# Kernel optimization log

Measured on AMD Instinct MI355X. Metric: run time of the kernel, lower is better.

Reference implementation:

```python
import jax, jax.numpy as jnp
import numpy as np

D_MODEL = 1024
N_HEADS = 16
D_HEAD = D_MODEL // N_HEADS
D_FF = 4096
EPS = 1e-5
NEG = -1e10


def setup_inputs() -> dict:
    key = jax.random.key(0)
    ks = jax.random.split(key, 16)
    s = 0.02
    x = jax.random.normal(ks[0], (4, 1024, D_MODEL), dtype=jnp.float32)
    mask = jnp.ones((4, 1, 1, 1024), dtype=jnp.int32)
    return {
        "x": x,
        "mask": mask,
        "Wq": jax.random.normal(ks[1], (D_MODEL, D_MODEL), jnp.float32) * s,
        "Wk": jax.random.normal(ks[2], (D_MODEL, D_MODEL), jnp.float32) * s,
        "Wv": jax.random.normal(ks[3], (D_MODEL, D_MODEL), jnp.float32) * s,
        "Wp": jax.random.normal(ks[4], (D_MODEL, D_MODEL), jnp.float32) * s,
        "bp": jnp.zeros((D_MODEL,), jnp.float32),
        "W1": jax.random.normal(ks[5], (D_MODEL, D_FF), jnp.float32) * s,
        "b1": jnp.zeros((D_FF,), jnp.float32),
        "W2": jax.random.normal(ks[6], (D_FF, D_MODEL), jnp.float32) * s,
        "b2": jnp.zeros((D_MODEL,), jnp.float32),
        "g1": jnp.ones((D_MODEL,), jnp.float32),
        "be1": jnp.zeros((D_MODEL,), jnp.float32),
        "g2": jnp.ones((D_MODEL,), jnp.float32),
        "be2": jnp.zeros((D_MODEL,), jnp.float32),
    }


def _layer_norm(x, g, b):
    mu = jnp.mean(x, axis=-1, keepdims=True)
    var = jnp.mean(jnp.square(x - mu), axis=-1, keepdims=True)
    return (x - mu) * jax.lax.rsqrt(var + EPS) * g + b


def _mha(x, mask, Wq, Wk, Wv, Wp, bp):
    B, L, _ = x.shape
    q = (x @ Wq).reshape(B, L, N_HEADS, D_HEAD).transpose(0, 2, 1, 3)  # (B,H,L,dh)
    k = (x @ Wk).reshape(B, L, N_HEADS, D_HEAD).transpose(0, 2, 1, 3)
    v = (x @ Wv).reshape(B, L, N_HEADS, D_HEAD).transpose(0, 2, 1, 3)
    scores = jnp.einsum('bhqd,bhkd->bhqk', q, k) / jnp.sqrt(jnp.float32(D_HEAD))
    scores = jnp.where(mask == 0, NEG, scores)
    attn = jax.nn.softmax(scores, axis=-1)
    heads = jnp.einsum('bhqk,bhkd->bhqd', attn, v)  # (B,H,L,dh)
    heads = heads.transpose(0, 2, 1, 3).reshape(B, L, D_MODEL)
    return heads @ Wp + bp


def reference(x, mask, Wq, Wk, Wv, Wp, bp, W1, b1, W2, b2, g1, be1, g2, be2):
    # Post-norm residual sublayers (dropout inactive at inference)
    attn_out = _mha(x, mask, Wq, Wk, Wv, Wp, bp)
    h = _layer_norm(x + attn_out, g1, be1)
    ff = jax.nn.relu(h @ W1 + b1) @ W2 + b2
    out = _layer_norm(h + ff, g2, be2)
    return out
```

## Files before the change

### kernel.cpp

```cpp
#include <hip/hip_runtime.h>
#include <hip/hip_bf16.h>

typedef __attribute__((ext_vector_type(8))) short short8;
typedef __attribute__((ext_vector_type(4))) short short4v;
typedef __attribute__((ext_vector_type(4))) float float4v;

static __device__ __forceinline__ float b2f(short s) {
    return __builtin_bit_cast(float, ((unsigned)(unsigned short)s) << 16);
}
static __device__ __forceinline__ short f2b(float f) {
    unsigned x = __builtin_bit_cast(unsigned, f);
    unsigned r = (x + 0x7fffu + ((x >> 16) & 1u)) >> 16;
    return (short)r;
}
static __device__ __forceinline__ void gload_lds16(const short* g, short* l) {
    __builtin_amdgcn_global_load_lds(
        (const __attribute__((address_space(1))) void*)g,
        (__attribute__((address_space(3))) void*)l, 16, 0, 0);
}

static __device__ __forceinline__ void tile_transpose(const float* __restrict__ in,
                                                      short* __restrict__ out,
                                                      int R, int C, int bx, int by,
                                                      float tile[64][65])
{
    const int tx = threadIdx.x;
    const int r0 = by * 64, c0 = bx * 64;
    const int lr = tx >> 4, lc = (tx & 15) * 4;
#pragma unroll
    for (int p = 0; p < 4; p++) {
        const float4v v = *(const float4v*)&in[(size_t)(r0 + lr + p * 16) * C + c0 + lc];
#pragma unroll
        for (int j = 0; j < 4; j++) tile[lr + p * 16][lc + j] = v[j];
    }
    __syncthreads();
    const int oc = tx >> 3, orr = (tx & 7) * 8;
#pragma unroll
    for (int p = 0; p < 2; p++) {
        const int c = oc + p * 32;
        short8 pk;
#pragma unroll
        for (int j = 0; j < 8; j++) pk[j] = f2b(tile[orr + j][c]);
        *(short8*)&out[(size_t)(c0 + c) * R + r0 + orr] = pk;
    }
}

__global__ __launch_bounds__(256) void prep_k(const float* __restrict__ x,
                                              const float* __restrict__ Wq,
                                              const float* __restrict__ Wk,
                                              const float* __restrict__ Wv,
                                              const float* __restrict__ Wp,
                                              const float* __restrict__ W1,
                                              const float* __restrict__ W2,
                                              short* __restrict__ xb,
                                              short* __restrict__ WqkvT,
                                              short* __restrict__ WpT,
                                              short* __restrict__ W1T,
                                              short* __restrict__ W2T)
{
    __shared__ float tile[64][65];
    const int b = blockIdx.x;
    if (b < 4096) {
        const size_t i = ((size_t)b * 256 + threadIdx.x) * 4;
        const float4v v = *(const float4v*)&x[i];
        short4v s;
#pragma unroll
        for (int j = 0; j < 4; j++) s[j] = f2b(v[j]);
        *(short4v*)&xb[i] = s;
    } else if (b < 5120) {
        const int lb = b - 4096;
        const int wsel = lb >> 8, t = lb & 255;
        const float* in = (wsel == 0) ? Wq : (wsel == 1) ? Wk : (wsel == 2) ? Wv : Wp;
        short* out = (wsel < 3) ? (WqkvT + ((size_t)wsel << 20)) : WpT;
        tile_transpose(in, out, 1024, 1024, t & 15, t >> 4, tile);
    } else if (b < 6144) {
        const int lb = b - 5120;
        tile_transpose(W1, W1T, 1024, 4096, lb & 63, lb >> 6, tile);
    } else {
        const int lb = b - 6144;
        tile_transpose(W2, W2T, 4096, 1024, lb & 15, lb >> 4, tile);
    }
}

template<int MODE, int BM, int BN, int KH>
__global__ __launch_bounds__(256) void gemm_bt(const short* __restrict__ X,
                                               const short* __restrict__ Wt,
                                               short* __restrict__ out,
                                               const float* __restrict__ bias,
                                               const short* __restrict__ alt,
                                               int M, int N, int K)
{
    constexpr int MI = BM / 32, NI = BN / 32;
    __shared__ short As[KH][BM * 32];
    __shared__ short Bs[KH][BN * 32];
    const int tid = threadIdx.x;
    const int wave = tid >> 6, lane = tid & 63;
    const int quad = lane >> 4, l16 = lane & 15;

    int bx = blockIdx.x, by = blockIdx.y;
    {
        const int nbx = gridDim.x, nby = gridDim.y;
        if ((nby & 7) == 0) {
            const int g = by * nbx + bx;
            const int xcd = g & 7, local = g >> 3, Y = nby >> 3;
            by = xcd * Y + (local % Y);
            bx = local / Y;
        }
    }
    const int m0 = by * BM, n0 = bx * BN;
    const int wm = (wave >> 1) * (BM / 2), wn = (wave & 1) * (BN / 2);

    int kb = 0, ke = K;
    short* op = out;
    if (MODE == 5) {
        const int ks = K / (int)gridDim.z;
        kb = blockIdx.z * ks;
        ke = kb + ks;
        op = (blockIdx.z == 3 && alt) ? const_cast<short*>(alt)
                                      : out + (size_t)blockIdx.z * M * N;
    }

    const int srow = tid >> 2;
    const int scs = (((tid & 3) ^ (srow & 3)) * 8);
    const int rg = ((l16 & 3)) * 8;

    float4v acc[MI][NI] = {};

    for (int k0 = kb; k0 < ke; k0 += KH * 32) {
#pragma unroll
        for (int c = 0; c < BM / 64; c++)
#pragma unroll
            for (int h = 0; h < KH; h++)
                gload_lds16(X + (size_t)(m0 + c * 64 + srow) * K + k0 + h * 32 + scs,
                            &As[h][(c * 256 + tid) * 8]);
#pragma unroll
        for (int c = 0; c < BN / 64; c++)
#pragma unroll
            for (int h = 0; h < KH; h++)
                gload_lds16(Wt + (size_t)(n0 + c * 64 + srow) * K + k0 + h * 32 + scs,
                            &Bs[h][(c * 256 + tid) * 8]);
        __syncthreads();
#pragma unroll
        for (int h = 0; h < KH; h++) {
            short8 af[MI], bf[NI];
#pragma unroll
            for (int i = 0; i < MI; i++)
                af[i] = *(const short8*)&As[h][(wm + i * 16 + l16) * 32 + ((quad * 8) ^ rg)];
#pragma unroll
            for (int i = 0; i < NI; i++)
                bf[i] = *(const short8*)&Bs[h][(wn + i * 16 + l16) * 32 + ((quad * 8) ^ rg)];
#pragma unroll
            for (int mi = 0; mi < MI; mi++)
#pragma unroll
                for (int ni = 0; ni < NI; ni++)
                    acc[mi][ni] = __builtin_amdgcn_mfma_f32_16x16x32_bf16(af[mi], bf[ni], acc[mi][ni], 0, 0, 0);
        }
        __syncthreads();
    }

#pragma unroll
    for (int mi = 0; mi < MI; mi++) {
#pragma unroll
        for (int ni = 0; ni < NI; ni++) {
            const int gn = n0 + wn + ni * 16 + l16;
            const float bv = (MODE == 2) ? bias[gn] : 0.0f;
#pragma unroll
            for (int r = 0; r < 4; r++) {
                const int gm = m0 + wm + mi * 16 + quad * 4 + r;
                float v = acc[mi][ni][r];
                if (MODE == 4) {
                    const int s = gn >> 10;
                    const int n = gn & 1023;
                    const int hh = n >> 6, d = n & 63;
                    const size_t bh16 = (size_t)((gm >> 10) * 16 + hh) << 16;
                    const size_t base = (size_t)s << 22;
                    if (s == 0)      out[base + bh16 + ((size_t)(gm & 1023) << 6) + d] = f2b(v * 0.125f);
                    else if (s == 1) out[base + bh16 + ((size_t)(gm & 1023) << 6) + d] = f2b(v);
                    else             out[base + bh16 + ((size_t)d << 10) + (gm & 1023)] = f2b(v);
                } else if (MODE == 2) {
                    v += bv;
                    v = fmaxf(v, 0.0f);
                    out[(size_t)gm * N + gn] = f2b(v);
                } else {
                    op[(size_t)gm * N + gn] = f2b(v);
                }
            }
        }
    }
}

__global__ __launch_bounds__(256) void attn_k(const short* __restrict__ Qb,
                                              const short* __restrict__ Kb,
                                              const short* __restrict__ Vt,
                                              const int* __restrict__ mask,
                                              short* __restrict__ heads)
{
    __shared__ short Kl[2][64 * 32];
    __shared__ short Vl[2][64 * 32];
    __shared__ short P[4][16 * 72];
    const int bh = blockIdx.x, qb = blockIdx.y;
    const int b = bh >> 4, h = bh & 15;
    const int tid = threadIdx.x, wave = tid >> 6, lane = tid & 63;
    const int quad = lane >> 4, l16 = lane & 15;
    const int qbase = qb * 64 + wave * 16;
    const short* Qp = Qb + ((size_t)bh << 16) + (size_t)qbase * 64;
    const short* Kp = Kb + ((size_t)bh << 16);
    const short* Vp = Vt + ((size_t)bh << 16);
    const int* mp = mask + (b << 10);

    const short8 bq0 = *(const short8*)&Qp[l16 * 64 + quad * 8];
    const short8 bq1 = *(const short8*)&Qp[l16 * 64 + 32 + quad * 8];

    float rs = 0.0f;
    float4v o[4] = {};
    short* myP = &P[wave][0];

    const int srow = tid >> 2, sc8 = (tid & 3) * 8;

    for (int kc = 0; kc < 1024; kc += 64) {
        gload_lds16(Kp + (size_t)(kc + srow) * 64 + sc8,      &Kl[0][tid * 8]);
        gload_lds16(Kp + (size_t)(kc + srow) * 64 + 32 + sc8, &Kl[1][tid * 8]);
        gload_lds16(Vp + (size_t)srow * 1024 + kc + sc8,      &Vl[0][tid * 8]);
        gload_lds16(Vp + (size_t)srow * 1024 + kc + 32 + sc8, &Vl[1][tid * 8]);
        __syncthreads();

        float4v s[4];
#pragma unroll
        for (int kt = 0; kt < 4; kt++) {
            s[kt] = (float4v){};
            const short8 ka = *(const short8*)&Kl[0][(kt * 16 + l16) * 32 + quad * 8];
            s[kt] = __builtin_amdgcn_mfma_f32_16x16x32_bf16(ka, bq0, s[kt], 0, 0, 0);
            const short8 kb = *(const short8*)&Kl[1][(kt * 16 + l16) * 32 + quad * 8];
            s[kt] = __builtin_amdgcn_mfma_f32_16x16x32_bf16(kb, bq1, s[kt], 0, 0, 0);
        }
#pragma unroll
        for (int kt = 0; kt < 4; kt++) {
            const int4 mv = *(const int4*)&mp[kc + kt * 16 + quad * 4];
            float p0 = mv.x ? __expf(fminf(s[kt][0], 30.f)) : 0.f;
            float p1 = mv.y ? __expf(fminf(s[kt][1], 30.f)) : 0.f;
            float p2 = mv.z ? __expf(fminf(s[kt][2], 30.f)) : 0.f;
            float p3 = mv.w ? __expf(fminf(s[kt][3], 30.f)) : 0.f;
            rs += (p0 + p1) + (p2 + p3);
            short4v w;
            w[0] = f2b(p0); w[1] = f2b(p1); w[2] = f2b(p2); w[3] = f2b(p3);
            *(short4v*)&myP[l16 * 72 + kt * 16 + quad * 4] = w;
        }
        const short8 bp0 = *(const short8*)&myP[l16 * 72 + quad * 8];
        const short8 bp1 = *(const short8*)&myP[l16 * 72 + 32 + quad * 8];
#pragma unroll
        for (int dt = 0; dt < 4; dt++) {
            const short8 va = *(const short8*)&Vl[0][(dt * 16 + l16) * 32 + quad * 8];
            o[dt] = __builtin_amdgcn_mfma_f32_16x16x32_bf16(va, bp0, o[dt], 0, 0, 0);
            const short8 vb = *(const short8*)&Vl[1][(dt * 16 + l16) * 32 + quad * 8];
            o[dt] = __builtin_amdgcn_mfma_f32_16x16x32_bf16(vb, bp1, o[dt], 0, 0, 0);
        }
        __syncthreads();
    }

    rs += __shfl_xor(rs, 16);
    rs += __shfl_xor(rs, 32);
    const float inv = 1.0f / fmaxf(rs, 1e-20f);
    const int gq = qbase + l16;
#pragma unroll
    for (int dt = 0; dt < 4; dt++) {
        short4v w;
#pragma unroll
        for (int r = 0; r < 4; r++) w[r] = f2b(o[dt][r] * inv);
        *(short4v*)&heads[((size_t)(b * 1024 + gq) << 10) + h * 64 + dt * 16 + quad * 4] = w;
    }
}

template<bool F32OUT>
__global__ __launch_bounds__(256) void red_ln_k(const short* __restrict__ p0,
                                                const short* __restrict__ p1,
                                                const short* __restrict__ p2,
                                                const short* __restrict__ p3,
                                                const float* __restrict__ bias,
                                                const short* __restrict__ res,
                                                const float* __restrict__ g,
                                                const float* __restrict__ be,
                                                short* __restrict__ outb,
                                                float* __restrict__ outf)
{
    __shared__ float red[8];
    const int row = blockIdx.x, tid = threadIdx.x;
    const size_t base = ((size_t)row << 10) + tid * 4;
    const short4v a = *(const short4v*)&p0[base];
    const short4v b = *(const short4v*)&p1[base];
    const short4v c = *(const short4v*)&p2[base];
    const short4v d = *(const short4v*)&p3[base];
    const short4v e = *(const short4v*)&res[base];
    const float4v bv = *(const float4v*)&bias[tid * 4];
    float v[4];
#pragma unroll
    for (int i = 0; i < 4; i++)
        v[i] = (b2f(a[i]) + b2f(b[i])) + (b2f(c[i]) + b2f(d[i])) + bv[i] + b2f(e[i]);
    float s = v[0] + v[1] + v[2] + v[3];
#pragma unroll
    for (int off = 32; off; off >>= 1) s += __shfl_xor(s, off);
    if ((tid & 63) == 0) red[tid >> 6] = s;
    __syncthreads();
    const float mu = (red[0] + red[1] + red[2] + red[3]) * (1.0f / 1024.0f);
    float vs = 0.f;
#pragma unroll
    for (int i = 0; i < 4; i++) { const float dd = v[i] - mu; vs += dd * dd; }
#pragma unroll
    for (int off = 32; off; off >>= 1) vs += __shfl_xor(vs, off);
    if ((tid & 63) == 0) red[4 + (tid >> 6)] = vs;
    __syncthreads();
    const float rstd = rsqrtf((red[4] + red[5] + red[6] + red[7]) * (1.0f / 1024.0f) + 1e-5f);
    const float4v gv = *(const float4v*)&g[tid * 4];
    const float4v bev = *(const float4v*)&be[tid * 4];
    if (F32OUT) {
        float4v w;
#pragma unroll
        for (int i = 0; i < 4; i++) w[i] = (v[i] - mu) * rstd * gv[i] + bev[i];
        *(float4v*)&outf[base] = w;
    } else {
        short4v w;
#pragma unroll
        for (int i = 0; i < 4; i++) w[i] = f2b((v[i] - mu) * rstd * gv[i] + bev[i]);
        *(short4v*)&outb[base] = w;
    }
}

extern "C" void kernel_launch(void* const* d_in, const int* in_sizes, int n_in,
                              void* d_out, int out_size, void* d_ws, size_t ws_size,
                              hipStream_t stream)
{
    const float* x   = (const float*)d_in[0];
    const int*   mk  = (const int*)d_in[1];
    const float* Wq  = (const float*)d_in[2];
    const float* Wk  = (const float*)d_in[3];
    const float* Wv  = (const float*)d_in[4];
    const float* Wp  = (const float*)d_in[5];
    const float* bp  = (const float*)d_in[6];
    const float* W1  = (const float*)d_in[7];
    const float* b1  = (const float*)d_in[8];
    const float* W2  = (const float*)d_in[9];
    const float* b2  = (const float*)d_in[10];
    const float* g1  = (const float*)d_in[11];
    const float* be1 = (const float*)d_in[12];
    const float* g2  = (const float*)d_in[13];
    const float* be2 = (const float*)d_in[14];
    float* out = (float*)d_out;

    char* ws = (char*)d_ws;
    const size_t MB = (size_t)1 << 20;
    short* xb     = (short*)(ws + 0 * MB);
    short* WqkvT  = (short*)(ws + 8 * MB);
    short* WpT    = (short*)(ws + 14 * MB);
    short* W1T    = (short*)(ws + 16 * MB);
    short* W2T    = (short*)(ws + 24 * MB);
    short* Qb     = (short*)(ws + 32 * MB);
    short* Kb     = (short*)(ws + 40 * MB);
    short* Vt     = (short*)(ws + 48 * MB);
    short* hd     = (short*)(ws + 56 * MB);
    short* partP  = (short*)(ws + 32 * MB);
    short* partP3 = (short*)(ws + 64 * MB);
    short* u      = (short*)(ws + 32 * MB);
    short* partF  = (short*)(ws + 0 * MB);
    short* partF3 = (short*)(ws + 64 * MB);
    short* hbuf   = (short*)(ws + 72 * MB);

    const dim3 blk(256);

    prep_k<<<dim3(7168), blk, 0, stream>>>(x, Wq, Wk, Wv, Wp, W1, W2,
                                           xb, WqkvT, WpT, W1T, W2T);

    gemm_bt<4, 128, 128, 2><<<dim3(24, 32), blk, 0, stream>>>(xb, WqkvT, Qb, nullptr, nullptr, 4096, 3072, 1024);

    attn_k<<<dim3(64, 16), blk, 0, stream>>>(Qb, Kb, Vt, mk, hd);

    gemm_bt<5, 128, 128, 2><<<dim3(8, 32, 4), blk, 0, stream>>>(hd, WpT, partP, nullptr, partP3, 4096, 1024, 1024);

    red_ln_k<false><<<dim3(4096), blk, 0, stream>>>(partP, partP + (4u << 20), partP + (8u << 20), partP3,
                                                    bp, xb, g1, be1, hbuf, nullptr);

    gemm_bt<2, 128, 128, 2><<<dim3(32, 32), blk, 0, stream>>>(hbuf, W1T, u, b1, nullptr, 4096, 4096, 1024);

    gemm_bt<5, 128, 128, 2><<<dim3(8, 32, 4), blk, 0, stream>>>(u, W2T, partF, nullptr, partF3, 4096, 1024, 4096);

    red_ln_k<true><<<dim3(4096), blk, 0, stream>>>(partF, partF + (4u << 20), partF + (8u << 20), partF3,
                                                   b2, hbuf, g2, be2, nullptr, out);
}
```

Measured before the change: 347.6 us.

## Prefetch next K/V tile into registers in attention; halve Wp split-K

The attention loop now issues global loads for the next K/V chunk into registers before computing on the current LDS tile, then writes them to LDS after the trailing barrier. This replaces direct global-to-LDS loads and is meant to overlap memory latency with the MFMA work. Separately, the output-projection GEMM uses a split-K of 2 instead of 4, and the reduce+layernorm kernel is templated on the number of partials so it reads only two partial buffers. The prefetch adds register pressure, and the smaller split reduces grid parallelism for that GEMM.

```diff
diff --git a/kernel.cpp b/kernel.cpp
--- a/kernel.cpp
+++ b/kernel.cpp
@@ -217,12 +217,23 @@
 
     const int srow = tid >> 2, sc8 = (tid & 3) * 8;
 
+    gload_lds16(Kp + (size_t)srow * 64 + sc8,        &Kl[0][tid * 8]);
+    gload_lds16(Kp + (size_t)srow * 64 + 32 + sc8,   &Kl[1][tid * 8]);
+    gload_lds16(Vp + (size_t)srow * 1024 + sc8,      &Vl[0][tid * 8]);
+    gload_lds16(Vp + (size_t)srow * 1024 + 32 + sc8, &Vl[1][tid * 8]);
+
     for (int kc = 0; kc < 1024; kc += 64) {
-        gload_lds16(Kp + (size_t)(kc + srow) * 64 + sc8,      &Kl[0][tid * 8]);
-        gload_lds16(Kp + (size_t)(kc + srow) * 64 + 32 + sc8, &Kl[1][tid * 8]);
-        gload_lds16(Vp + (size_t)srow * 1024 + kc + sc8,      &Vl[0][tid * 8]);
-        gload_lds16(Vp + (size_t)srow * 1024 + kc + 32 + sc8, &Vl[1][tid * 8]);
         __syncthreads();
+
+        short8 nk0, nk1, nv0, nv1;
+        const bool pf = (kc + 64) < 1024;
+        if (pf) {
+            const int kn = kc + 64;
+            nk0 = *(const short8*)&Kp[(size_t)(kn + srow) * 64 + sc8];
+            nk1 = *(const short8*)&Kp[(size_t)(kn + srow) * 64 + 32 + sc8];
+            nv0 = *(const short8*)&Vp[(size_t)srow * 1024 + kn + sc8];
+            nv1 = *(const short8*)&Vp[(size_t)srow * 1024 + kn + 32 + sc8];
+        }
 
         float4v s[4];
 #pragma unroll
@@ -254,7 +265,14 @@
             const short8 vb = *(const short8*)&Vl[1][(dt * 16 + l16) * 32 + quad * 8];
             o[dt] = __builtin_amdgcn_mfma_f32_16x16x32_bf16(vb, bp1, o[dt], 0, 0, 0);
         }
+
         __syncthreads();
+        if (pf) {
+            *(short8*)&Kl[0][tid * 8] = nk0;
+            *(short8*)&Kl[1][tid * 8] = nk1;
+            *(short8*)&Vl[0][tid * 8] = nv0;
+            *(short8*)&Vl[1][tid * 8] = nv1;
+        }
     }
 
     rs += __shfl_xor(rs, 16);
@@ -270,7 +288,7 @@
     }
 }
 
-template<bool F32OUT>
+template<int NP, bool F32OUT>
 __global__ __launch_bounds__(256) void red_ln_k(const short* __restrict__ p0,
                                                 const short* __restrict__ p1,
                                                 const short* __restrict__ p2,
@@ -287,14 +305,17 @@
     const size_t base = ((size_t)row << 10) + tid * 4;
     const short4v a = *(const short4v*)&p0[base];
     const short4v b = *(const short4v*)&p1[base];
-    const short4v c = *(const short4v*)&p2[base];
-    const short4v d = *(const short4v*)&p3[base];
     const short4v e = *(const short4v*)&res[base];
     const float4v bv = *(const float4v*)&bias[tid * 4];
     float v[4];
 #pragma unroll
-    for (int i = 0; i < 4; i++)
-        v[i] = (b2f(a[i]) + b2f(b[i])) + (b2f(c[i]) + b2f(d[i])) + bv[i] + b2f(e[i]);
+    for (int i = 0; i < 4; i++) v[i] = b2f(a[i]) + b2f(b[i]) + bv[i] + b2f(e[i]);
+    if constexpr (NP == 4) {
+        const short4v c = *(const short4v*)&p2[base];
+        const short4v d = *(const short4v*)&p3[base];
+#pragma unroll
+        for (int i = 0; i < 4; i++) v[i] += b2f(c[i]) + b2f(d[i]);
+    }
     float s = v[0] + v[1] + v[2] + v[3];
 #pragma unroll
     for (int off = 32; off; off >>= 1) s += __shfl_xor(s, off);
@@ -357,7 +378,6 @@
     short* Vt     = (short*)(ws + 48 * MB);
     short* hd     = (short*)(ws + 56 * MB);
     short* partP  = (short*)(ws + 32 * MB);
-    short* partP3 = (short*)(ws + 64 * MB);
     short* u      = (short*)(ws + 32 * MB);
     short* partF  = (short*)(ws + 0 * MB);
     short* partF3 = (short*)(ws + 64 * MB);
@@ -372,15 +392,15 @@
 
     attn_k<<<dim3(64, 16), blk, 0, stream>>>(Qb, Kb, Vt, mk, hd);
 
-    gemm_bt<5, 128, 128, 2><<<dim3(8, 32, 4), blk, 0, stream>>>(hd, WpT, partP, nullptr, partP3, 4096, 1024, 1024);
-
-    red_ln_k<false><<<dim3(4096), blk, 0, stream>>>(partP, partP + (4u << 20), partP + (8u << 20), partP3,
-                                                    bp, xb, g1, be1, hbuf, nullptr);
+    gemm_bt<5, 128, 128, 2><<<dim3(8, 32, 2), blk, 0, stream>>>(hd, WpT, partP, nullptr, nullptr, 4096, 1024, 1024);
+
+    red_ln_k<2, false><<<dim3(4096), blk, 0, stream>>>(partP, partP + (4u << 20), nullptr, nullptr,
+                                                       bp, xb, g1, be1, hbuf, nullptr);
 
     gemm_bt<2, 128, 128, 2><<<dim3(32, 32), blk, 0, stream>>>(hbuf, W1T, u, b1, nullptr, 4096, 4096, 1024);
 
     gemm_bt<5, 128, 128, 2><<<dim3(8, 32, 4), blk, 0, stream>>>(u, W2T, partF, nullptr, partF3, 4096, 1024, 4096);
 
-    red_ln_k<true><<<dim3(4096), blk, 0, stream>>>(partF, partF + (4u << 20), partF + (8u << 20), partF3,
-                                                   b2, hbuf, g2, be2, nullptr, out);
-}
+    red_ln_k<4, true><<<dim3(4096), blk, 0, stream>>>(partF, partF + (4u << 20), partF + (8u << 20), partF3,
+                                                      b2, hbuf, g2, be2, nullptr, out);
+}
```

Result: no change. 342.6 us (-1.5%).
